# Kernel tuning notes

Hardware: AMD Instinct MI355X
Metric: run time of the kernel (lower is better)

## Reference

```python
import jax, jax.numpy as jnp
import numpy as np
from jax import lax

GROUPS = 32
CH = 2048
CG = CH // GROUPS  # 64 channels per group
H = W = 64
B = 4
EPS = 1e-5


def _conv2d(x, w, b, padding, dilation=1):
    # x: [N, Cin, H, W], w: [Cout, Cin, kh, kw] (OIHW)
    y = lax.conv_general_dilated(
        x, w, window_strides=(1, 1),
        padding=[(padding, padding), (padding, padding)],
        rhs_dilation=(dilation, dilation),
        dimension_numbers=("NCHW", "OIHW", "NCHW"))
    return y + b[None, :, None, None]


def _prelu(x, alpha):
    # single shared slope (num_parameters=1)
    return jnp.where(x >= 0, x, alpha[0] * x)


def setup_inputs() -> dict:
    key = jax.random.key(0)
    ks = jax.random.split(key, 6)
    s = 0.05
    f32 = jnp.float32
    return {
        "x": jax.random.normal(ks[0], (B, CH, H, W), f32),
        # EFFM.conv1x1 (on concatenated pooled h/w strips)
        "w_hw": jax.random.normal(ks[1], (CG, CG, 1, 1), f32) * s,
        "b_hw": jnp.zeros((CG,), f32),
        # GroupNorm(cg, cg): per-channel affine
        "gn_w": jnp.ones((CG,), f32),
        "gn_b": jnp.zeros((CG,), f32),
        # RC branch1: 3x3 conv pad=1 + PReLU
        "w_b1": jax.random.normal(ks[2], (CG, CG, 3, 3), f32) * s,
        "b_b1": jnp.zeros((CG,), f32),
        "a_b1": jnp.full((1,), 0.25, f32),
        # RC branch2: 3x3 conv dilation=2 pad=2 + PReLU
        "w_b2": jax.random.normal(ks[3], (CG, CG, 3, 3), f32) * s,
        "b_b2": jnp.zeros((CG,), f32),
        "a_b2": jnp.full((1,), 0.25, f32),
        # RC conv128to64: 1x1 conv 2*cg -> cg
        "w_cat": jax.random.normal(ks[4], (CG, 2 * CG, 1, 1), f32) * s,
        "b_cat": jnp.zeros((CG,), f32),
    }


def _effm(x, w_hw, b_hw, gn_w, gn_b, w_b1, b_b1, a_b1, w_b2, b_b2, a_b2, w_cat, b_cat):
    b, c, h, w = x.shape
    cg = c // GROUPS
    bg = b * GROUPS
    gx = x.reshape(bg, cg, h, w)

    # --- coordinate attention branch ---
    x_h = jnp.mean(gx, axis=3, keepdims=True)                       # [bg, cg, h, 1]
    x_w = jnp.mean(gx, axis=2, keepdims=True).transpose(0, 1, 3, 2)  # [bg, cg, w, 1]
    hw = jnp.concatenate([x_h, x_w], axis=2)                         # [bg, cg, h+w, 1]
    # 1x1 conv == channel mixing linear
    hw = jnp.einsum("oi,bilk->bolk", w_hw[:, :, 0, 0], hw) + b_hw[None, :, None, None]
    x_h, x_w = hw[:, :, :h, :], hw[:, :, h:, :]
    gate = gx * jax.nn.sigmoid(x_h) * jax.nn.sigmoid(x_w.transpose(0, 1, 3, 2))

    # GroupNorm(num_groups=cg, num_channels=cg) == per-channel instance norm
    mu = jnp.mean(gate, axis=(2, 3), keepdims=True)
    var = jnp.var(gate, axis=(2, 3), keepdims=True)
    x1 = (gate - mu) * lax.rsqrt(var + EPS)
    x1 = x1 * gn_w[None, :, None, None] + gn_b[None, :, None, None]

    # --- RC multi-scale branch ---
    br1 = _prelu(_conv2d(gx, w_b1, b_b1, padding=1), a_b1) + gx
    br2 = _prelu(_conv2d(gx, w_b2, b_b2, padding=2, dilation=2), a_b2) + gx
    cat = jnp.concatenate([br1, br2], axis=1)                        # [bg, 2cg, h, w]
    x2 = jnp.einsum("oi,bihw->bohw", w_cat[:, :, 0, 0], cat) + b_cat[None, :, None, None]

    # --- cross softmax-matmul attention ---
    x11 = jax.nn.softmax(jnp.mean(x1, axis=(2, 3)), axis=-1)          # [bg, cg]
    x21 = jax.nn.softmax(jnp.mean(x2, axis=(2, 3)), axis=-1)          # [bg, cg]
    weights = (jnp.einsum("gc,gchw->ghw", x11, x2)
               + jnp.einsum("gc,gchw->ghw", x21, x1))                # [bg, h, w]
    out = gx * jax.nn.sigmoid(weights)[:, None, :, :]
    return out.reshape(b, c, h, w)


def reference(x, w_hw, b_hw, gn_w, gn_b, w_b1, b_b1, a_b1, w_b2, b_b2, a_b2, w_cat, b_cat):
    return _effm(x, w_hw, b_hw, gn_w, gn_b, w_b1, b_b1, a_b1, w_b2, b_b2, a_b2, w_cat, b_cat)
```

## Files before the change

### kernel.cpp

```cpp
#include <hip/hip_runtime.h>
#include <hip/hip_bf16.h>

#define HWPX 4096

typedef __attribute__((ext_vector_type(8))) short short8v;
typedef __attribute__((ext_vector_type(4))) float f32x4;
typedef __attribute__((ext_vector_type(16))) float f32x16;
#define MFMA32(a,b,c) __builtin_amdgcn_mfma_f32_32x32x16_bf16(a,b,c,0,0,0)

__device__ __forceinline__ float sigf(float x){ return 1.0f/(1.0f+__expf(-x)); }
__device__ __forceinline__ unsigned short f2bf(float f){
  __hip_bfloat16 h = __float2bfloat16(f);
  unsigned short u; __builtin_memcpy(&u, &h, sizeof(u)); return u;
}
__device__ __forceinline__ float bf2f(unsigned short u){
  return __uint_as_float(((unsigned)u)<<16);
}
__device__ __forceinline__ void gl2lds16(const void* g, void* l){
  __builtin_amdgcn_global_load_lds((const __attribute__((address_space(1))) void*)g,
                                   (__attribute__((address_space(3))) void*)l, 16, 0, 0);
}

__global__ __launch_bounds__(256) void k_pre(const float* __restrict__ x,
                                             const float* __restrict__ wb1,
                                             const float* __restrict__ wb2,
                                             const float* __restrict__ wcat,
                                             const float* __restrict__ gnb,
                                             unsigned short* __restrict__ xb,
                                             float* __restrict__ hwbuf,
                                             unsigned short* __restrict__ wimg,
                                             unsigned short* __restrict__ wcimg,
                                             float* __restrict__ x11,
                                             float* __restrict__ x2mean){
  int bid = blockIdx.x, tid = threadIdx.x;
  if (bid >= 1088){
    int idx = (bid - 1088)*2048 + tid*8;
    f32x4 z = {0.f,0.f,0.f,0.f};
    *(f32x4*)(x2mean + idx) = z;
    *(f32x4*)(x2mean + idx + 4) = z;
    return;
  }
  if (bid >= 1024){
    int bid2 = bid - 1024;
    for (int idx = bid2*256 + tid; idx < 73728; idx += 64*256){
      int f = idx >> 9, r = idx & 511, lane = r >> 3, j = r & 7;
      int qc = f / 36, rem = f % 36, tap = rem >> 2, kc = rem & 3;
      int q = qc >> 1, conv = qc & 1, kf = kc >> 1, cot = kc & 1;
      int co = cot*32 + (lane & 31);
      int ci = q*32 + kf*16 + (lane >> 5)*8 + j;
      const float* src = conv ? wb2 : wb1;
      wimg[idx] = f2bf(src[(co*64 + ci)*9 + tap]);
    }
    if (bid2 == 0){
      for (int idx = tid; idx < 8192; idx += 256){
        int f = idx >> 9, r = idx & 511, lane = r >> 3, j = r & 7;
        int kfc = f >> 1, cot = f & 1;
        int o = cot*32 + (lane & 31);
        int ch = kfc*16 + (lane >> 5)*8 + j;
        wcimg[idx] = f2bf(wcat[o*128 + ch]);
      }
      if (tid < 64){
        float g = gnb[tid];
        float m = g;
        for (int s=32; s; s>>=1) m = fmaxf(m, __shfl_xor(m, s));
        float e = __expf(g-m);
        float se = e;
        for (int s=32; s; s>>=1) se += __shfl_xor(se, s);
        x11[tid] = e/se;
      }
    }
    return;
  }
  int g = bid >> 3, slot = bid & 7;
  int col = tid & 63, wid = tid >> 6;
  __shared__ float rsm[8*64];
  __shared__ float csm[4*8*64];
  float colacc[8] = {0,0,0,0,0,0,0,0};
  const float* xbase = x + ((size_t)(g*64 + slot*8))*HWPX;
  for (int p=0;p<16;++p){
    int r = wid + 4*p;
    const float* src = xbase + r*64 + col;
    float v[8];
    #pragma unroll
    for (int e=0;e<8;e++) v[e] = src[(size_t)e*HWPX];
    unsigned pk[4];
    #pragma unroll
    for (int j=0;j<4;j++) pk[j] = (unsigned)f2bf(v[2*j]) | ((unsigned)f2bf(v[2*j+1])<<16);
    f32x4 st; __builtin_memcpy(&st, pk, 16);
    *(f32x4*)((char*)xb + (((size_t)(g*64+r))*8 + slot)*1024 + col*16) = st;
    #pragma unroll
    for (int e=0;e<8;e++){
      float s = v[e];
      s += __shfl_xor(s,1); s += __shfl_xor(s,2); s += __shfl_xor(s,4);
      s += __shfl_xor(s,8); s += __shfl_xor(s,16); s += __shfl_xor(s,32);
      if ((tid&63)==0) rsm[e*64+r] = s;
      colacc[e] += v[e];
    }
  }
  #pragma unroll
  for (int e=0;e<8;e++) csm[(wid*8+e)*64+col] = colacc[e];
  __syncthreads();
  float* hb = hwbuf + ((size_t)(g*64 + slot*8))*128;
  for (int idx=tid; idx<512; idx+=256){
    int e = idx>>6, r = idx&63;
    hb[e*128 + r] = rsm[e*64+r] * (1.0f/64.0f);
  }
  for (int idx=tid; idx<512; idx+=256){
    int e = idx>>6, c2 = idx&63;
    float s = csm[(0*8+e)*64+c2] + csm[(1*8+e)*64+c2] + csm[(2*8+e)*64+c2] + csm[(3*8+e)*64+c2];
    hb[e*128 + 64 + c2] = s * (1.0f/64.0f);
  }
}

__global__ __launch_bounds__(256) void k_hwmm(const float* hwbuf, const float* whw,
                                              const float* bhw, float* sigbuf){
  int g = blockIdx.x;
  __shared__ float hl[64*128];
  int tid = threadIdx.x;
  const float* src = hwbuf + (size_t)g*8192;
  for (int i = tid; i < 2048; i += 256) ((float4*)hl)[i] = ((const float4*)src)[i];
  __syncthreads();
  int p  = tid & 127;
  int o0 = (tid >> 7) * 32;
  float acc[32];
  #pragma unroll
  for (int k=0;k<32;k++) acc[k] = bhw[o0+k];
  for (int i=0;i<64;i++){
    float v = hl[i*128+p];
    #pragma unroll
    for (int k=0;k<32;k++) acc[k] = fmaf(whw[(o0+k)*64+i], v, acc[k]);
  }
  float* dst = sigbuf + (size_t)g*8192;
  #pragma unroll
  for (int k=0;k<32;k++) dst[(o0+k)*128+p] = sigf(acc[k]);
}

__global__ __launch_bounds__(256) void k_gate2(const unsigned short* __restrict__ xb,
                                               const float* __restrict__ sigbuf,
                                               const float* __restrict__ gnw,
                                               const float* __restrict__ gnb,
                                               float* __restrict__ scsh){
  int bsw = (blockIdx.x & 7)*(gridDim.x >> 3) + (blockIdx.x >> 3);
  int g = bsw >> 3, slot = bsw & 7;
  int tid = threadIdx.x, col = tid & 63, wq = tid >> 6, lane = tid & 63;
  __shared__ float srm[8*64], scm[8*64], red[4*16];
  for (int idx = tid; idx < 1024; idx += 256){
    int e = idx >> 7, k = idx & 127;
    float v = sigbuf[(size_t)g*8192 + (size_t)(slot*8+e)*128 + k];
    if (k < 64) srm[e*64+k] = v; else scm[e*64+k-64] = v;
  }
  __syncthreads();
  float s[8] = {0,0,0,0,0,0,0,0}, s2[8] = {0,0,0,0,0,0,0,0};
  const char* base = (const char*)xb + (((size_t)(g*64))*8 + slot)*1024;
  for (int p=0;p<16;++p){
    int row = wq*16 + p;
    short8v xv = *(const short8v*)(base + (size_t)row*8192 + col*16);
    #pragma unroll
    for (int e=0;e<8;e++){
      float v = bf2f((unsigned short)xv[e]) * srm[e*64+row] * scm[e*64+col];
      s[e] += v; s2[e] = fmaf(v, v, s2[e]);
    }
  }
  #pragma unroll
  for (int e=0;e<8;e++){
    #pragma unroll
    for (int off=1; off<64; off<<=1){ s[e] += __shfl_xor(s[e], off); s2[e] += __shfl_xor(s2[e], off); }
  }
  if (lane == 0){
    #pragma unroll
    for (int e=0;e<8;e++){ red[wq*16+e] = s[e]; red[wq*16+8+e] = s2[e]; }
  }
  __syncthreads();
  if (tid < 8){
    float S  = red[tid]   + red[16+tid] + red[32+tid] + red[48+tid];
    float S2 = red[8+tid] + red[24+tid] + red[40+tid] + red[56+tid];
    float mu = S*(1.f/4096.f);
    float var = S2*(1.f/4096.f) - mu*mu;
    int c = slot*8 + tid;
    float scale = rsqrtf(var + 1e-5f) * gnw[c];
    scsh[(g*64+c)*2]   = scale;
    scsh[(g*64+c)*2+1] = gnb[c] - mu*scale;
  }
}

template<int DIL>
__device__ __forceinline__ void conv_compute(const char* INq, const char* wq,
                                             int ch2, int rquad, int l31, int lh, int lane,
                                             f32x16 acc[2][4]){
  constexpr int NROW = 4 + 2*DIL;
  #pragma unroll
  for (int kf=0; kf<2; ++kf){
    #pragma unroll
    for (int dxx=0; dxx<3; ++dxx){
      const int colb = ch2*32 + l31 + (dxx-1)*DIL + 2;
      short8v Brow[NROW];
      #pragma unroll
      for (int i=0; i<NROW; ++i){
        int rowi = rquad*4 + i + 2 - DIL;
        Brow[i] = *(const short8v*)(INq + (rowi*4 + kf*2 + lh)*1088 + colb*16);
      }
      #pragma unroll
      for (int dyy=0; dyy<3; ++dyy){
        int tap = dyy*3 + dxx;
        const char* wp = wq + (size_t)(tap*4 + kf*2)*1024 + lane*16;
        short8v A0 = *(const short8v*)(wp);
        short8v A1 = *(const short8v*)(wp + 1024);
        #pragma unroll
        for (int pt=0; pt<4; ++pt){
          acc[0][pt] = MFMA32(A0, Brow[pt + dyy*DIL], acc[0][pt]);
          acc[1][pt] = MFMA32(A1, Brow[pt + dyy*DIL], acc[1][pt]);
        }
      }
    }
  }
}

__global__ __launch_bounds__(512) void k_convcat(const unsigned short* __restrict__ xb,
                                                 const char* __restrict__ wgl,
                                                 const char* __restrict__ wcgl,
                                                 const float* __restrict__ bb1,
                                                 const float* __restrict__ bb2,
                                                 const float* __restrict__ a1p,
                                                 const float* __restrict__ a2p,
                                                 const float* __restrict__ bcat,
                                                 const float* __restrict__ x11,
                                                 float* __restrict__ wsum2,
                                                 float* __restrict__ x2mean){
  extern __shared__ char smem[];
  char* BRL = smem;
  float* x11l = (float*)(smem + 131072);
  float* bcl  = x11l + 64;

  const int tid = threadIdx.x;
  const int bsw = (blockIdx.x & 7)*(gridDim.x >> 3) + (blockIdx.x >> 3);
  const int g = bsw >> 3;
  const int strip = bsw & 7;
  const int r0 = strip*8;
  const int w = tid >> 6;
  const int lane = tid & 63;
  const int l31 = lane & 31;
  const int lh  = lane >> 5;
  const int conv = w >> 2;
  const int ch2 = (w >> 1) & 1;
  const int rquad = w & 1;

  if (tid < 64){ x11l[tid] = x11[tid]; bcl[tid] = bcat[tid]; }
  if (tid < 384){
    int b = tid / 192, t = tid % 192;
    int seg = t >> 2, pc = t & 3;
    int colp = (pc < 2) ? pc : pc + 64;
    *(f32x4*)(smem + b*52224 + seg*1088 + colp*16) = (f32x4){0.f,0.f,0.f,0.f};
  }

  #pragma unroll
  for (int i=0;i<6;++i){
    int seg = w*6 + i;
    int row = seg >> 2, slot = seg & 3;
    int rg = r0 - 2 + row;
    char* dst = smem + seg*1088 + 32;
    if ((unsigned)rg < 64u){
      const char* src = (const char*)xb + ((((size_t)(g*64+rg))*8) + slot)*1024 + lane*16;
      gl2lds16(src, dst + lane*16);
    } else {
      *(f32x4*)(dst + lane*16) = (f32x4){0.f,0.f,0.f,0.f};
    }
  }

  f32x16 acc[2][4];
  #pragma unroll
  for (int cot=0;cot<2;cot++)
    #pragma unroll
    for (int pt=0;pt<4;pt++)
      #pragma unroll
      for (int e=0;e<16;e++) acc[cot][pt][e] = 0.f;

  __syncthreads();

  #pragma unroll
  for (int i=0;i<6;++i){
    int seg = w*6 + i;
    int row = seg >> 2, slot = seg & 3;
    int rg = r0 - 2 + row;
    char* dst = smem + 52224 + seg*1088 + 32;
    if ((unsigned)rg < 64u){
      const char* src = (const char*)xb + ((((size_t)(g*64+rg))*8) + 4 + slot)*1024 + lane*16;
      gl2lds16(src, dst + lane*16);
    } else {
      *(f32x4*)(dst + lane*16) = (f32x4){0.f,0.f,0.f,0.f};
    }
  }

  {
    const char* wq = wgl + (size_t)((0*2 + conv)*9*4)*1024;
    if (conv == 0) conv_compute<1>(smem, wq, ch2, rquad, l31, lh, lane, acc);
    else           conv_compute<2>(smem, wq, ch2, rquad, l31, lh, lane, acc);
  }
  __syncthreads();

  {
    const char* wq = wgl + (size_t)((1*2 + conv)*9*4)*1024;
    if (conv == 0) conv_compute<1>(smem + 52224, wq, ch2, rquad, l31, lh, lane, acc);
    else           conv_compute<2>(smem + 52224, wq, ch2, rquad, l31, lh, lane, acc);
  }
  __syncthreads();

  {
    const float alpha = conv ? a2p[0] : a1p[0];
    const float* bbp = conv ? bb2 : bb1;
    #pragma unroll
    for (int cot=0;cot<2;++cot){
      #pragma unroll
      for (int rq=0;rq<4;++rq){
        int co0 = cot*32 + 8*rq + 4*lh;
        float b0 = bbp[co0], b1 = bbp[co0+1], b2 = bbp[co0+2], b3 = bbp[co0+3];
        int ch0 = conv*64 + co0;
        #pragma unroll
        for (int pt=0;pt<4;++pt){
          int prow = rquad*4 + pt;
          int colg = ch2*32 + l31;
          const char* rsrc = (const char*)xb + (((size_t)(g*64 + r0 + prow))*8 + (co0>>3))*1024
                             + colg*16 + (co0&7)*2;
          ushort4 rv = *(const ushort4*)rsrc;
          float v0 = acc[cot][pt][rq*4+0] + b0; v0 = (v0>=0.f? v0 : alpha*v0) + bf2f(rv.x);
          float v1 = acc[cot][pt][rq*4+1] + b1; v1 = (v1>=0.f? v1 : alpha*v1) + bf2f(rv.y);
          float v2 = acc[cot][pt][rq*4+2] + b2; v2 = (v2>=0.f? v2 : alpha*v2) + bf2f(rv.z);
          float v3 = acc[cot][pt][rq*4+3] + b3; v3 = (v3>=0.f? v3 : alpha*v3) + bf2f(rv.w);
          int px = prow*64 + colg;
          int addr = (px*256 + ch0*2) ^ ((px & 15) << 4);
          ushort4 pk; pk.x=f2bf(v0); pk.y=f2bf(v1); pk.z=f2bf(v2); pk.w=f2bf(v3);
          *(ushort4*)(BRL + addr) = pk;
        }
      }
    }
  }
  __syncthreads();

  {
    f32x16 c2[2][2];
    #pragma unroll
    for (int cot=0;cot<2;cot++)
      #pragma unroll
      for (int t=0;t<2;t++)
        #pragma unroll
        for (int e=0;e<16;e++) c2[cot][t][e] = 0.f;

    #pragma unroll
    for (int kfc=0;kfc<8;++kfc){
      const char* ap = wcgl + (size_t)(kfc*2)*1024 + lane*16;
      short8v A0 = *(const short8v*)(ap);
      short8v A1 = *(const short8v*)(ap + 1024);
      #pragma unroll
      for (int t=0;t<2;++t){
        int px = w*64 + t*32 + l31;
        int addr = (px*256 + kfc*32 + lh*16) ^ ((px & 15) << 4);
        short8v B = *(const short8v*)(BRL + addr);
        c2[0][t] = MFMA32(A0, B, c2[0][t]);
        c2[1][t] = MFMA32(A1, B, c2[1][t]);
      }
    }
    float u0 = 0.f, u1 = 0.f;
    #pragma unroll
    for (int cot=0;cot<2;++cot){
      #pragma unroll
      for (int reg=0;reg<16;++reg){
        int o = cot*32 + (reg&3) + 8*(reg>>2) + 4*lh;
        float xw = x11l[o], bc = bcl[o];
        u0 += xw*(c2[cot][0][reg] + bc);
        u1 += xw*(c2[cot][1][reg] + bc);
        float sv = c2[cot][0][reg] + c2[cot][1][reg];
        sv += __shfl_xor(sv, 1); sv += __shfl_xor(sv, 2);
        sv += __shfl_xor(sv, 4); sv += __shfl_xor(sv, 8); sv += __shfl_xor(sv, 16);
        if (l31 == 0) atomicAdd(&x2mean[g*64 + o], sv);
      }
    }
    u0 += __shfl_xor(u0, 32);
    u1 += __shfl_xor(u1, 32);
    if (lh == 0){
      float* wp2 = wsum2 + (size_t)g*4096 + strip*512 + w*64 + l31;
      wp2[0]  = u0;
      wp2[32] = u1;
    }
  }
}

__global__ __launch_bounds__(256) void k_final2(const float* __restrict__ x,
                                                const float* __restrict__ sigbuf,
                                                const float* __restrict__ scsh,
                                                const float* __restrict__ x2mean,
                                                const float* __restrict__ bcat,
                                                const float* __restrict__ wsum2,
                                                float* __restrict__ out){
  int blk = blockIdx.x;
  int g = blk >> 4, chunk = blk & 15;
  int tid = threadIdx.x;
  __shared__ float x21s[64];
  __shared__ float crow[64*4];
  __shared__ float ccol[64*64];
  __shared__ float Ssm;
  const float* sgb = sigbuf + (size_t)g*8192;
  if (tid < 64){
    float mean = x2mean[g*64 + tid] * (1.f/4096.f) + bcat[tid];
    float mx = mean;
    for (int s=32; s; s>>=1) mx = fmaxf(mx, __shfl_xor(mx, s));
    float e = __expf(mean - mx);
    float se = e;
    for (int s=32; s; s>>=1) se += __shfl_xor(se, s);
    x21s[tid] = e/se;
  }
  for (int idx = tid; idx < 4096; idx += 256){
    int c = idx >> 6, col = idx & 63;
    ccol[idx] = sgb[c*128 + 64 + col];
  }
  __syncthreads();
  {
    int c = tid >> 2, rr = tid & 3;
    crow[tid] = x21s[c] * scsh[(g*64+c)*2] * sgb[c*128 + chunk*4 + rr];
  }
  if (tid < 64){
    float v = x21s[tid] * scsh[(g*64+tid)*2+1];
    for (int s=32; s; s>>=1) v += __shfl_xor(v, s);
    if (tid == 0) Ssm = v;
  }
  __syncthreads();
  int px = chunk*256 + tid;
  int rr = tid >> 6, col = tid & 63;
  const float* xp = x + (size_t)(g*64)*HWPX + px;
  float W = wsum2[(size_t)g*4096 + px] + Ssm;
  float xv[64];
  #pragma unroll
  for (int c=0;c<64;c++){
    xv[c] = xp[(size_t)c*HWPX];
    W = fmaf(crow[c*4+rr]*ccol[c*64+col], xv[c], W);
  }
  float s = sigf(W);
  float* op = out + (size_t)(g*64)*HWPX + px;
  #pragma unroll
  for (int c=0;c<64;c++){
    op[(size_t)c*HWPX] = xv[c] * s;
  }
}

extern "C" void kernel_launch(void* const* d_in, const int* in_sizes, int n_in,
                              void* d_out, int out_size, void* d_ws, size_t ws_size,
                              hipStream_t stream) {
  const float* x     = (const float*)d_in[0];
  const float* w_hw  = (const float*)d_in[1];
  const float* b_hw  = (const float*)d_in[2];
  const float* gn_w  = (const float*)d_in[3];
  const float* gn_b  = (const float*)d_in[4];
  const float* w_b1  = (const float*)d_in[5];
  const float* b_b1  = (const float*)d_in[6];
  const float* a_b1  = (const float*)d_in[7];
  const float* w_b2  = (const float*)d_in[8];
  const float* b_b2  = (const float*)d_in[9];
  const float* a_b2  = (const float*)d_in[10];
  const float* w_cat = (const float*)d_in[11];
  const float* b_cat = (const float*)d_in[12];

  char* ws = (char*)d_ws;
  unsigned short* wimg  = (unsigned short*)(ws + 0);
  unsigned short* wcimg = (unsigned short*)(ws + 147456);
  float* x11    = (float*)(ws + 163840);
  float* x2mean = (float*)(ws + 164096);
  float* scsh   = (float*)(ws + 196864);
  float* wsum2  = (float*)(ws + 262400);
  float* hwbuf  = (float*)(ws + 2359552);
  float* sigb   = (float*)(ws + 6553856);
  unsigned short* xb = (unsigned short*)d_out;
  float* out = (float*)d_out;

  hipFuncSetAttribute(reinterpret_cast<const void*>(k_convcat),
                      hipFuncAttributeMaxDynamicSharedMemorySize, 131584);

  k_pre  <<<1092, 256, 0, stream>>>(x, w_b1, w_b2, w_cat, gn_b, xb, hwbuf, wimg, wcimg,
                                    x11, x2mean);
  k_hwmm <<<128,  256, 0, stream>>>(hwbuf, w_hw, b_hw, sigb);
  k_gate2<<<1024, 256, 0, stream>>>(xb, sigb, gn_w, gn_b, scsh);
  k_convcat<<<1024, 512, 131584, stream>>>(xb, (const char*)wimg, (const char*)wcimg,
                                           b_b1, b_b2, a_b1, a_b2, b_cat, x11, wsum2, x2mean);
  k_final2<<<2048, 256, 0, stream>>>(x, sigb, scsh, x2mean, b_cat, wsum2, out);
}
```

Measured before the change: 303.4 us.

## Stage conv weights in LDS and double-buffer four 16-channel input chunks

The conv-cat kernel now splits the 64 input channels into four 16-channel chunks. Each chunk's input rows and its bf16 weight image are loaded into LDS, and the loads are double-buffered so the next chunk's fetch overlaps the current chunk's MFMA work. Conv weights used to be read straight from global memory; they are now read from LDS, and the weight image is reordered in the prep kernel to match. The 1x1 cat weights are also staged in LDS. In exchange, LDS use grows to about 148KB and there are more barriers per block.

```diff
diff --git a/kernel.cpp b/kernel.cpp
--- a/kernel.cpp
+++ b/kernel.cpp
@@ -44,10 +44,11 @@
     int bid2 = bid - 1024;
     for (int idx = bid2*256 + tid; idx < 73728; idx += 64*256){
       int f = idx >> 9, r = idx & 511, lane = r >> 3, j = r & 7;
-      int qc = f / 36, rem = f % 36, tap = rem >> 2, kc = rem & 3;
-      int q = qc >> 1, conv = qc & 1, kf = kc >> 1, cot = kc & 1;
+      int ck = f / 36, rem = f % 36;
+      int conv = rem / 18, rem2 = rem % 18;
+      int tap = rem2 >> 1, cot = rem2 & 1;
       int co = cot*32 + (lane & 31);
-      int ci = q*32 + kf*16 + (lane >> 5)*8 + j;
+      int ci = ck*16 + (lane >> 5)*8 + j;
       const float* src = conv ? wb2 : wb1;
       wimg[idx] = f2bf(src[(co*64 + ci)*9 + tap]);
     }
@@ -184,32 +185,30 @@
 }
 
 template<int DIL>
-__device__ __forceinline__ void conv_compute(const char* INq, const char* wq,
+__device__ __forceinline__ void conv_compute(const char* INq, const char* WLq,
                                              int ch2, int rquad, int l31, int lh, int lane,
                                              f32x16 acc[2][4]){
   constexpr int NROW = 4 + 2*DIL;
-  #pragma unroll
-  for (int kf=0; kf<2; ++kf){
-    #pragma unroll
-    for (int dxx=0; dxx<3; ++dxx){
-      const int colb = ch2*32 + l31 + (dxx-1)*DIL + 2;
-      short8v Brow[NROW];
-      #pragma unroll
-      for (int i=0; i<NROW; ++i){
-        int rowi = rquad*4 + i + 2 - DIL;
-        Brow[i] = *(const short8v*)(INq + (rowi*4 + kf*2 + lh)*1088 + colb*16);
-      }
-      #pragma unroll
-      for (int dyy=0; dyy<3; ++dyy){
-        int tap = dyy*3 + dxx;
-        const char* wp = wq + (size_t)(tap*4 + kf*2)*1024 + lane*16;
-        short8v A0 = *(const short8v*)(wp);
-        short8v A1 = *(const short8v*)(wp + 1024);
-        #pragma unroll
-        for (int pt=0; pt<4; ++pt){
-          acc[0][pt] = MFMA32(A0, Brow[pt + dyy*DIL], acc[0][pt]);
-          acc[1][pt] = MFMA32(A1, Brow[pt + dyy*DIL], acc[1][pt]);
-        }
+  constexpr int conv = DIL - 1;
+  #pragma unroll
+  for (int dxx=0; dxx<3; ++dxx){
+    const int colb = ch2*32 + l31 + (dxx-1)*DIL + 2;
+    short8v Brow[NROW];
+    #pragma unroll
+    for (int i=0; i<NROW; ++i){
+      int rowi = rquad*4 + i + 2 - DIL;
+      Brow[i] = *(const short8v*)(INq + (rowi*2 + lh)*1088 + colb*16);
+    }
+    #pragma unroll
+    for (int dyy=0; dyy<3; ++dyy){
+      int tap = dyy*3 + dxx;
+      const char* wp = WLq + (size_t)((conv*9 + tap)*2)*1024 + lane*16;
+      short8v A0 = *(const short8v*)(wp);
+      short8v A1 = *(const short8v*)(wp + 1024);
+      #pragma unroll
+      for (int pt=0; pt<4; ++pt){
+        acc[0][pt] = MFMA32(A0, Brow[pt + dyy*DIL], acc[0][pt]);
+        acc[1][pt] = MFMA32(A1, Brow[pt + dyy*DIL], acc[1][pt]);
       }
     }
   }
@@ -228,7 +227,8 @@
                                                  float* __restrict__ x2mean){
   extern __shared__ char smem[];
   char* BRL = smem;
-  float* x11l = (float*)(smem + 131072);
+  char* WCL = smem + 131072;
+  float* x11l = (float*)(smem + 147456);
   float* bcl  = x11l + 64;
 
   const int tid = threadIdx.x;
@@ -245,25 +245,16 @@
   const int rquad = w & 1;
 
   if (tid < 64){ x11l[tid] = x11[tid]; bcl[tid] = bcat[tid]; }
-  if (tid < 384){
-    int b = tid / 192, t = tid % 192;
+  if (tid < 192){
+    int b = tid / 96, t = tid % 96;
     int seg = t >> 2, pc = t & 3;
     int colp = (pc < 2) ? pc : pc + 64;
-    *(f32x4*)(smem + b*52224 + seg*1088 + colp*16) = (f32x4){0.f,0.f,0.f,0.f};
-  }
-
-  #pragma unroll
-  for (int i=0;i<6;++i){
-    int seg = w*6 + i;
-    int row = seg >> 2, slot = seg & 3;
-    int rg = r0 - 2 + row;
-    char* dst = smem + seg*1088 + 32;
-    if ((unsigned)rg < 64u){
-      const char* src = (const char*)xb + ((((size_t)(g*64+rg))*8) + slot)*1024 + lane*16;
-      gl2lds16(src, dst + lane*16);
-    } else {
-      *(f32x4*)(dst + lane*16) = (f32x4){0.f,0.f,0.f,0.f};
-    }
+    *(f32x4*)(smem + b*26112 + seg*1088 + colp*16) = (f32x4){0.f,0.f,0.f,0.f};
+  }
+  #pragma unroll
+  for (int k=0;k<2;k++){
+    int idx = tid + k*512;
+    gl2lds16(wcgl + (size_t)idx*16, WCL + idx*16);
   }
 
   f32x16 acc[2][4];
@@ -274,35 +265,43 @@
       #pragma unroll
       for (int e=0;e<16;e++) acc[cot][pt][e] = 0.f;
 
-  __syncthreads();
-
-  #pragma unroll
-  for (int i=0;i<6;++i){
-    int seg = w*6 + i;
-    int row = seg >> 2, slot = seg & 3;
-    int rg = r0 - 2 + row;
-    char* dst = smem + 52224 + seg*1088 + 32;
-    if ((unsigned)rg < 64u){
-      const char* src = (const char*)xb + ((((size_t)(g*64+rg))*8) + 4 + slot)*1024 + lane*16;
-      gl2lds16(src, dst + lane*16);
-    } else {
-      *(f32x4*)(dst + lane*16) = (f32x4){0.f,0.f,0.f,0.f};
-    }
-  }
-
-  {
-    const char* wq = wgl + (size_t)((0*2 + conv)*9*4)*1024;
-    if (conv == 0) conv_compute<1>(smem, wq, ch2, rquad, l31, lh, lane, acc);
-    else           conv_compute<2>(smem, wq, ch2, rquad, l31, lh, lane, acc);
-  }
-  __syncthreads();
-
-  {
-    const char* wq = wgl + (size_t)((1*2 + conv)*9*4)*1024;
-    if (conv == 0) conv_compute<1>(smem + 52224, wq, ch2, rquad, l31, lh, lane, acc);
-    else           conv_compute<2>(smem + 52224, wq, ch2, rquad, l31, lh, lane, acc);
-  }
-  __syncthreads();
+  auto stage_chunk = [&](int ck, char* inb, char* wb){
+    #pragma unroll
+    for (int k=0;k<4;k++){
+      int idx = tid + k*512;
+      gl2lds16(wgl + (size_t)ck*36864 + (size_t)idx*16, wb + idx*16);
+    }
+    if (tid < 256){
+      int idx = 2048 + tid;
+      gl2lds16(wgl + (size_t)ck*36864 + (size_t)idx*16, wb + idx*16);
+    }
+    #pragma unroll
+    for (int i=0;i<3;++i){
+      int seg = w*3 + i;
+      int row = seg >> 1, slot = seg & 1;
+      int rg = r0 - 2 + row;
+      char* dst = inb + seg*1088 + 32 + lane*16;
+      if ((unsigned)rg < 64u){
+        gl2lds16((const char*)xb + (((size_t)(g*64+rg))*8 + ck*2 + slot)*1024 + lane*16, dst);
+      } else {
+        *(f32x4*)dst = (f32x4){0.f,0.f,0.f,0.f};
+      }
+    }
+  };
+
+  stage_chunk(0, smem, smem + 52224);
+  __syncthreads();
+
+  #pragma unroll
+  for (int ck=0; ck<4; ++ck){
+    if (ck < 3)
+      stage_chunk(ck+1, smem + ((ck+1)&1)*26112, smem + 52224 + ((ck+1)&1)*36864);
+    const char* inq = smem + (ck&1)*26112;
+    const char* wq  = smem + 52224 + (ck&1)*36864;
+    if (conv == 0) conv_compute<1>(inq, wq, ch2, rquad, l31, lh, lane, acc);
+    else           conv_compute<2>(inq, wq, ch2, rquad, l31, lh, lane, acc);
+    __syncthreads();
+  }
 
   {
     const float alpha = conv ? a2p[0] : a1p[0];
@@ -346,7 +345,7 @@
 
     #pragma unroll
     for (int kfc=0;kfc<8;++kfc){
-      const char* ap = wcgl + (size_t)(kfc*2)*1024 + lane*16;
+      const char* ap = WCL + (size_t)(kfc*2)*1024 + lane*16;
       short8v A0 = *(const short8v*)(ap);
       short8v A1 = *(const short8v*)(ap + 1024);
       #pragma unroll
@@ -470,13 +469,13 @@
   float* out = (float*)d_out;
 
   hipFuncSetAttribute(reinterpret_cast<const void*>(k_convcat),
-                      hipFuncAttributeMaxDynamicSharedMemorySize, 131584);
+                      hipFuncAttributeMaxDynamicSharedMemorySize, 147968);
 
   k_pre  <<<1092, 256, 0, stream>>>(x, w_b1, w_b2, w_cat, gn_b, xb, hwbuf, wimg, wcimg,
                                     x11, x2mean);
   k_hwmm <<<128,  256, 0, stream>>>(hwbuf, w_hw, b_hw, sigb);
   k_gate2<<<1024, 256, 0, stream>>>(xb, sigb, gn_w, gn_b, scsh);
-  k_convcat<<<1024, 512, 131584, stream>>>(xb, (const char*)wimg, (const char*)wcimg,
+  k_convcat<<<1024, 512, 147968, stream>>>(xb, (const char*)wimg, (const char*)wcimg,
                                            b_b1, b_b2, a_b1, a_b2, b_cat, x11, wsum2, x2mean);
   k_final2<<<2048, 256, 0, stream>>>(x, sigb, scsh, x2mean, b_cat, wsum2, out);
 }
```

New measurement: 287.4 us. -5.3%, faster.
